# Kernel optimization log

Measured on AMD Instinct MI355X. Metric: run time of the kernel, lower is better.

## Reference

```python
import jax, jax.numpy as jnp
import numpy as np

B = 4096          # graphs per batch
SENSORS = 9       # nodes per graph (9*8 = 72 directed edges = 36 pairs x 2)
PAIRS = 36
E_PER_G = 72
HID = 3.0  # unused marker
H = 128
L = 4
EPS = 1e-8


def _build_edge_index():
    # 36 unordered pairs (i<j); per pair emit (i->j) then (j->i) so that
    # reshape(B, 36, 2) groups the two directions of each pair together.
    pairs = [(i, j) for i in range(SENSORS) for j in range(i + 1, SENSORS)]
    rows, cols = [], []
    for i, j in pairs:
        rows += [i, j]
        cols += [j, i]
    rows = np.asarray(rows, np.int32)
    cols = np.asarray(cols, np.int32)
    offs = (np.arange(B, dtype=np.int32) * SENSORS)[:, None]  # [B,1]
    row = (rows[None, :] + offs).reshape(-1)
    col = (cols[None, :] + offs).reshape(-1)
    return jnp.asarray(np.stack([row, col]))  # [2, B*72]


def setup_inputs() -> dict:
    key = jax.random.key(0)
    ks = iter(jax.random.split(key, 32))
    N = B * SENSORS

    def lin(k, fin, fout):
        s = 1.0 / np.sqrt(fin)
        kw, kb = jax.random.split(k)
        return (jax.random.uniform(kw, (fin, fout), jnp.float32, -s, s),
                jax.random.uniform(kb, (fout,), jnp.float32, -s, s))

    x_nodes = jax.random.normal(next(ks), (N, 2), jnp.float32)
    damage_locs = jax.random.normal(next(ks), (B, 2), jnp.float32)
    edge_index = _build_edge_index()
    node_batch = jnp.repeat(jnp.arange(B, dtype=jnp.int32), SENSORS)

    enc_n_w, enc_n_b = lin(next(ks), 2, H)
    enc_e_w1, enc_e_b1 = lin(next(ks), 6, H)
    enc_e_w2, enc_e_b2 = lin(next(ks), H, H)

    ew1, eb1, ew2, eb2, nw1, nb1, nw2, nb2 = [], [], [], [], [], [], [], []
    for _ in range(L):
        w, b = lin(next(ks), 3 * H, H); ew1.append(w); eb1.append(b)
        w, b = lin(next(ks), H, H);     ew2.append(w); eb2.append(b)
        w, b = lin(next(ks), 2 * H, H); nw1.append(w); nb1.append(b)
        w, b = lin(next(ks), H, H);     nw2.append(w); nb2.append(b)
    stk = lambda xs: jnp.stack(xs)

    dec_w1, dec_b1 = lin(next(ks), H, H // 2)
    dec_w2, dec_b2 = lin(next(ks), H // 2, 1)

    return dict(
        x_nodes=x_nodes, damage_locs=damage_locs,
        enc_n_w=enc_n_w, enc_n_b=enc_n_b,
        enc_e_w1=enc_e_w1, enc_e_b1=enc_e_b1, enc_e_w2=enc_e_w2, enc_e_b2=enc_e_b2,
        edge_w1=stk(ew1), edge_b1=stk(eb1), edge_w2=stk(ew2), edge_b2=stk(eb2),
        node_w1=stk(nw1), node_b1=stk(nb1), node_w2=stk(nw2), node_b2=stk(nb2),
        dec_w1=dec_w1, dec_b1=dec_b1, dec_w2=dec_w2, dec_b2=dec_b2,
        edge_index=edge_index, node_batch=node_batch,
    )


def _forward(x_nodes, damage_locs,
             enc_n_w, enc_n_b, enc_e_w1, enc_e_b1, enc_e_w2, enc_e_b2,
             edge_w1, edge_b1, edge_w2, edge_b2,
             node_w1, node_b1, node_w2, node_b2,
             dec_w1, dec_b1, dec_w2, dec_b2,
             edge_index, node_batch):
    N = x_nodes.shape[0]
    row, col = edge_index[0], edge_index[1]
    src = x_nodes[row]                      # [E,2] sender coords (p1)
    dst = x_nodes[col]                      # [E,2] receiver coords (p2)
    dmg = damage_locs[node_batch[row]]      # [E,2] (p3)

    vec = src - dst
    edge_len = jnp.sqrt(jnp.sum(vec * vec, -1, keepdims=True) + EPS)
    d21 = dst - src
    l2 = jnp.clip(jnp.sum(d21 * d21, -1, keepdims=True), EPS, None)
    t = jnp.clip(jnp.sum((dmg - src) * d21, -1, keepdims=True) / l2, 0.0, 1.0)
    proj = src + t * d21
    d_path = jnp.sqrt(jnp.sum((dmg - proj) ** 2, -1, keepdims=True) + EPS)
    d_tx = jnp.sqrt(jnp.sum((src - dmg) ** 2, -1, keepdims=True) + EPS)
    d_rx = jnp.sqrt(jnp.sum((dst - dmg) ** 2, -1, keepdims=True) + EPS)
    phys = jnp.concatenate([vec, edge_len, d_path, d_tx, d_rx], axis=1)  # [E,6]

    h_n = x_nodes @ enc_n_w + enc_n_b
    h_e = jax.nn.relu(phys @ enc_e_w1 + enc_e_b1) @ enc_e_w2 + enc_e_b2

    ones = jnp.ones((row.shape[0],), h_n.dtype)
    deg = jnp.clip(jax.ops.segment_sum(ones, col, num_segments=N), 1.0, None)[:, None]

    for l in range(L):
        ein = jnp.concatenate([h_n[row], h_n[col], h_e], axis=1)  # [E,3H]
        h_e = h_e + jax.nn.relu(ein @ edge_w1[l] + edge_b1[l]) @ edge_w2[l] + edge_b2[l]
        # PyG default message(x_j): mean of sender node features at receiver
        agg = jax.ops.segment_sum(h_n[row], col, num_segments=N) / deg
        nin = jnp.concatenate([h_n, agg], axis=1)                 # [N,2H]
        h_n = h_n + jax.nn.relu(nin @ node_w1[l] + node_b1[l]) @ node_w2[l] + node_b2[l]

    dec = jax.nn.sigmoid(jax.nn.relu(h_e @ dec_w1 + dec_b1) @ dec_w2 + dec_b2)  # [E,1]
    return dec.reshape(B, PAIRS, 2).mean(axis=2)  # [B,36]


def reference(x_nodes, damage_locs,
              enc_n_w, enc_n_b, enc_e_w1, enc_e_b1, enc_e_w2, enc_e_b2,
              edge_w1, edge_b1, edge_w2, edge_b2,
              node_w1, node_b1, node_w2, node_b2,
              dec_w1, dec_b1, dec_w2, dec_b2,
              edge_index, node_batch):
    return _forward(x_nodes, damage_locs,
                    enc_n_w, enc_n_b, enc_e_w1, enc_e_b1, enc_e_w2, enc_e_b2,
                    edge_w1, edge_b1, edge_w2, edge_b2,
                    node_w1, node_b1, node_w2, node_b2,
                    dec_w1, dec_b1, dec_w2, dec_b2,
                    edge_index, node_batch)
```

## Files before the change

kernel.cpp:

```cpp
#include <hip/hip_runtime.h>
#include <math.h>

typedef unsigned short u16;
typedef __attribute__((ext_vector_type(8))) short bf16x8;
typedef __attribute__((ext_vector_type(4))) float f32x4;

#define NSENS 9
#define NEDGE 72
#define NPAIR 36
#define HDIM 128
#define NLAYER 4
#define FEPS 1e-8f

#define ST    136
#define STNIN 264
#define STPH  40

__device__ __forceinline__ u16 f2bf(float f) {
    unsigned u = __float_as_uint(f);
    return (u16)((u + 0x7FFFu + ((u >> 16) & 1u)) >> 16);
}
__device__ __forceinline__ float bf2f(u16 h) { return __uint_as_float(((unsigned)h) << 16); }

__device__ __forceinline__ unsigned cvt2(float lo, float hi) {
#if defined(__has_builtin)
#if __has_builtin(__builtin_amdgcn_cvt_pk_bf16_f32)
    typedef __attribute__((ext_vector_type(2))) __bf16 bf16x2_t;
    bf16x2_t t = __builtin_amdgcn_cvt_pk_bf16_f32(lo, hi);
    unsigned u; __builtin_memcpy(&u, &t, 4); return u;
#else
    return ((unsigned)f2bf(hi) << 16) | (unsigned)f2bf(lo);
#endif
#else
    return ((unsigned)f2bf(hi) << 16) | (unsigned)f2bf(lo);
#endif
}

#define SZ_EE1 (1*8*512)
#define SZ_EE2 (4*8*512)
#define SZ_EW1 (12*8*512)
#define SZ_EW2 (4*8*512)
#define SZ_NW1 (8*8*512)
#define SZ_NW2 (4*8*512)
#define SZ_DW1 (4*4*512)
#define OFF_EE1 0
#define OFF_EE2 (OFF_EE1 + SZ_EE1)
#define OFF_EW1 (OFF_EE2 + SZ_EE2)
#define OFF_EW2 (OFF_EW1 + 4*SZ_EW1)
#define OFF_NW1 (OFF_EW2 + 4*SZ_EW2)
#define OFF_NW2 (OFF_NW1 + 4*SZ_NW1)
#define OFF_DW1 (OFF_NW2 + 4*SZ_NW2)

__device__ __forceinline__ void pack_one(const float* __restrict__ s, u16* __restrict__ d,
                                         int Ksrc, int N, int NT, int kbnt) {
    const int kb = kbnt / NT, nt = kbnt % NT;
    const int ln = threadIdx.x, q = ln >> 4, c = ln & 15;
    const int n  = nt * 16 + c;
    u16* dp = d + ((kb * NT + nt) * 64 + ln) * 8;
#pragma unroll
    for (int j = 0; j < 8; ++j) {
        int k = kb * 32 + q * 8 + j;
        dp[j] = f2bf((k < Ksrc) ? s[k * N + n] : 0.f);
    }
}

__global__ void pack_all(const float* __restrict__ ee1, const float* __restrict__ ee2,
                         const float* __restrict__ ew1, const float* __restrict__ ew2,
                         const float* __restrict__ nw1, const float* __restrict__ nw2,
                         const float* __restrict__ dw1, u16* __restrict__ ws) {
    int b = blockIdx.x;
    if (b < 8)        { pack_one(ee1, ws + OFF_EE1, 6, 128, 8, b); return; }
    b -= 8;
    if (b < 32)       { pack_one(ee2, ws + OFF_EE2, 128, 128, 8, b); return; }
    b -= 32;
    if (b < 384)      { int l = b / 96;
                        pack_one(ew1 + l*384*128, ws + OFF_EW1 + l*SZ_EW1, 384, 128, 8, b % 96); return; }
    b -= 384;
    if (b < 128)      { int l = b / 32;
                        pack_one(ew2 + l*128*128, ws + OFF_EW2 + l*SZ_EW2, 128, 128, 8, b % 32); return; }
    b -= 128;
    if (b < 256)      { int l = b / 64;
                        pack_one(nw1 + l*256*128, ws + OFF_NW1 + l*SZ_NW1, 256, 128, 8, b % 64); return; }
    b -= 256;
    if (b < 128)      { int l = b / 32;
                        pack_one(nw2 + l*128*128, ws + OFF_NW2 + l*SZ_NW2, 128, 128, 8, b % 32); return; }
    b -= 128;
    pack_one(dw1, ws + OFF_DW1, 128, 64, 4, b);
}

template<int NMT, int NKB, int NT, typename FA>
__device__ __forceinline__ void wave_gemm(const u16* __restrict__ Wp, int nt, int ln,
                                          FA fa, f32x4* acc) {
    const u16* wp = Wp + (nt * 64 + ln) * 8;
    bf16x8 bc = *(const bf16x8*)(wp);
#pragma unroll
    for (int kb = 0; kb < NKB; ++kb) {
        bf16x8 bn;
        if (kb + 1 < NKB) bn = *(const bf16x8*)(wp + (kb + 1) * NT * 512);
#pragma unroll
        for (int mt = 0; mt < NMT; ++mt) {
            bf16x8 a = fa(mt, kb);
            acc[mt] = __builtin_amdgcn_mfma_f32_16x16x32_bf16(a, bc, acc[mt], 0, 0, 0);
        }
        if (kb + 1 < NKB) bc = bn;
    }
}

#define BACC(A, N, b) do { _Pragma("unroll") for (int _i = 0; _i < (N); ++_i) \
                           (A)[_i] = (f32x4){(b), (b), (b), (b)}; } while (0)

extern "C" __global__ void __launch_bounds__(512, 2)
gnn_mfma(const float* __restrict__ x_nodes, const float* __restrict__ damage_locs,
         const float* __restrict__ enc_n_w, const float* __restrict__ enc_n_b,
         const float* __restrict__ enc_e_b1, const float* __restrict__ enc_e_b2,
         const float* __restrict__ edge_b1, const float* __restrict__ edge_b2,
         const float* __restrict__ node_b1, const float* __restrict__ node_b2,
         const float* __restrict__ dec_b1, const float* __restrict__ dec_w2,
         const float* __restrict__ dec_b2,
         const u16* __restrict__ wpack, float* __restrict__ out)
{
    __shared__ __align__(16) u16 smem[176 * ST];
    __shared__ float s_x[NSENS * 2];
    __shared__ float s_dmg[2];
    __shared__ float s_val[NEDGE];
    __shared__ int s_src[NEDGE], s_dst[NEDGE];

    u16* b_he  = smem;
    u16* b_t   = smem + 80 * ST;
    u16* b_hn  = smem + 160 * ST;
    u16* b_ph  = b_he;
    u16* b_nin = b_t;
    u16* b_nt  = b_t + 48 * ST;

    const int g   = blockIdx.x;
    const int tid = threadIdx.x;
    const int wv  = tid >> 6, ln = tid & 63;
    const int q   = ln >> 4,  cl = ln & 15;
    const int col = wv * 16 + cl;

    auto st4 = [&](u16* buf, int stride, int c, int Rb, int Rlim,
                   float v0, float v1, float v2, float v3) {
        unsigned d01 = cvt2(v0, v1), d23 = cvt2(v2, v3);
        if (Rb + 0 < Rlim) buf[(Rb + 0) * stride + c] = (u16)d01;
        if (Rb + 1 < Rlim) buf[(Rb + 1) * stride + c] = (u16)(d01 >> 16);
        if (Rb + 2 < Rlim) buf[(Rb + 2) * stride + c] = (u16)d23;
        if (Rb + 3 < Rlim) buf[(Rb + 3) * stride + c] = (u16)(d23 >> 16);
    };

    {
        uint4 z = {0, 0, 0, 0};
        uint4* zp = (uint4*)b_ph;
        for (int i = tid; i < (80 * STPH * 2) / 16; i += 512) zp[i] = z;
    }
    if (tid < NSENS * 2) s_x[tid] = x_nodes[g * NSENS * 2 + tid];
    if (tid < 2)         s_dmg[tid] = damage_locs[g * 2 + tid];
    if (tid < NEDGE) {
        int p = tid >> 1;
        int i = 0, rem = p, cnt = 8;
        while (rem >= cnt) { rem -= cnt; --cnt; ++i; }
        int j = i + 1 + rem;
        s_src[tid] = (tid & 1) ? j : i;
        s_dst[tid] = (tid & 1) ? i : j;
    }
    __syncthreads();

    if (tid < NEDGE) {
        const int si = s_src[tid], di = s_dst[tid];
        const float sx = s_x[2*si], sy = s_x[2*si+1];
        const float dx = s_x[2*di], dy = s_x[2*di+1];
        const float gx = s_dmg[0],  gy = s_dmg[1];
        const float vx = sx - dx, vy = sy - dy;
        const float vv = vx*vx + vy*vy;
        const float elen = sqrtf(vv + FEPS);
        const float l2 = fmaxf(vv, FEPS);
        float t = ((gx - sx) * (dx - sx) + (gy - sy) * (dy - sy)) / l2;
        t = fminf(fmaxf(t, 0.f), 1.f);
        const float px = sx + t * (dx - sx), py = sy + t * (dy - sy);
        u16* ph = b_ph + tid * STPH;
        ph[0] = f2bf(vx); ph[1] = f2bf(vy); ph[2] = f2bf(elen);
        ph[3] = f2bf(sqrtf((gx-px)*(gx-px) + (gy-py)*(gy-py) + FEPS));
        ph[4] = f2bf(sqrtf((sx-gx)*(sx-gx) + (sy-gy)*(sy-gy) + FEPS));
        ph[5] = f2bf(sqrtf((dx-gx)*(dx-gx) + (dy-gy)*(dy-gy) + FEPS));
    }

    f32x4 m_hn;
    {
        const float w0 = enc_n_w[col], w1 = enc_n_w[HDIM + col], bb = enc_n_b[col];
#pragma unroll
        for (int r = 0; r < 4; ++r) {
            const int R = q * 4 + r;
            m_hn[r] = (R < NSENS) ? fmaf(s_x[2*R], w0, fmaf(s_x[2*R+1], w1, bb)) : 0.f;
        }
        st4(b_hn, ST, col, q * 4, NSENS, m_hn[0], m_hn[1], m_hn[2], m_hn[3]);
    }

    int rowS[5], rowD[5], rowE[5];
#pragma unroll
    for (int mt = 0; mt < 5; ++mt) {
        int e = mt * 16 + cl; if (e >= NEDGE) e = NEDGE - 1;
        rowS[mt] = s_src[e] * ST; rowD[mt] = s_dst[e] * ST; rowE[mt] = e * ST;
    }
    __syncthreads();

    auto fa_t   = [&](int mt, int kb) -> bf16x8 {
        return *(const bf16x8*)(b_t + (mt * 16 + cl) * ST + kb * 32 + q * 8); };
    auto fa_ph  = [&](int mt, int kb) -> bf16x8 {
        return *(const bf16x8*)(b_ph + (mt * 16 + cl) * STPH + q * 8); };
    auto fa_nin = [&](int mt, int kb) -> bf16x8 {
        return *(const bf16x8*)(b_nin + cl * STNIN + kb * 32 + q * 8); };
    auto fa_nt  = [&](int mt, int kb) -> bf16x8 {
        return *(const bf16x8*)(b_nt + cl * ST + kb * 32 + q * 8); };
    auto fa_ein = [&](int mt, int kb) -> bf16x8 {
        const u16* p;
        if (kb < 4)      p = b_hn + rowS[mt] + kb * 32;
        else if (kb < 8) p = b_hn + rowD[mt] + (kb - 4) * 32;
        else             p = b_he + rowE[mt] + (kb - 8) * 32;
        return *(const bf16x8*)(p + q * 8); };

    f32x4 m_he[5];

    {
        f32x4 acc[5]; BACC(acc, 5, enc_e_b1[col]);
        wave_gemm<5, 1, 8>(wpack + OFF_EE1, wv, ln, fa_ph, acc);
#pragma unroll
        for (int mt = 0; mt < 5; ++mt)
            st4(b_t, ST, col, mt * 16 + q * 4, NEDGE,
                fmaxf(acc[mt][0], 0.f), fmaxf(acc[mt][1], 0.f),
                fmaxf(acc[mt][2], 0.f), fmaxf(acc[mt][3], 0.f));
    }
    __syncthreads();
    {
        f32x4 acc[5]; BACC(acc, 5, enc_e_b2[col]);
        wave_gemm<5, 4, 8>(wpack + OFF_EE2, wv, ln, fa_t, acc);
#pragma unroll
        for (int mt = 0; mt < 5; ++mt) {
            m_he[mt] = acc[mt];
            st4(b_he, ST, col, mt * 16 + q * 4, NEDGE,
                m_he[mt][0], m_he[mt][1], m_he[mt][2], m_he[mt][3]);
        }
    }
    __syncthreads();

    for (int l = 0; l < NLAYER; ++l) {
        {
            f32x4 acc[5]; BACC(acc, 5, edge_b1[l * HDIM + col]);
            wave_gemm<5, 12, 8>(wpack + OFF_EW1 + l * SZ_EW1, wv, ln, fa_ein, acc);
#pragma unroll
            for (int mt = 0; mt < 5; ++mt)
                st4(b_t, ST, col, mt * 16 + q * 4, NEDGE,
                    fmaxf(acc[mt][0], 0.f), fmaxf(acc[mt][1], 0.f),
                    fmaxf(acc[mt][2], 0.f), fmaxf(acc[mt][3], 0.f));
        }
        __syncthreads();
        {
            f32x4 acc[5]; BACC(acc, 5, edge_b2[l * HDIM + col]);
            wave_gemm<5, 4, 8>(wpack + OFF_EW2 + l * SZ_EW2, wv, ln, fa_t, acc);
#pragma unroll
            for (int mt = 0; mt < 5; ++mt) {
#pragma unroll
                for (int r = 0; r < 4; ++r) m_he[mt][r] += acc[mt][r];
                st4(b_he, ST, col, mt * 16 + q * 4, NEDGE,
                    m_he[mt][0], m_he[mt][1], m_he[mt][2], m_he[mt][3]);
            }
        }
        __syncthreads();
        {
            float p4 = m_hn[0] + m_hn[1] + m_hn[2] + m_hn[3];
            p4 += __shfl_xor(p4, 16);
            p4 += __shfl_xor(p4, 32);
            st4(b_nin, STNIN, col, q * 4, NSENS, m_hn[0], m_hn[1], m_hn[2], m_hn[3]);
            st4(b_nin, STNIN, HDIM + col, q * 4, NSENS,
                (p4 - m_hn[0]) * 0.125f, (p4 - m_hn[1]) * 0.125f,
                (p4 - m_hn[2]) * 0.125f, (p4 - m_hn[3]) * 0.125f);
        }
        __syncthreads();
        {
            f32x4 acc[1]; BACC(acc, 1, node_b1[l * HDIM + col]);
            wave_gemm<1, 8, 8>(wpack + OFF_NW1 + l * SZ_NW1, wv, ln, fa_nin, acc);
            st4(b_nt, ST, col, q * 4, 16,
                fmaxf(acc[0][0], 0.f), fmaxf(acc[0][1], 0.f),
                fmaxf(acc[0][2], 0.f), fmaxf(acc[0][3], 0.f));
        }
        __syncthreads();
        {
            f32x4 acc[1]; BACC(acc, 1, node_b2[l * HDIM + col]);
            wave_gemm<1, 4, 8>(wpack + OFF_NW2 + l * SZ_NW2, wv, ln, fa_nt, acc);
#pragma unroll
            for (int r = 0; r < 4; ++r)
                if (q * 4 + r < NSENS) m_hn[r] += acc[0][r];
            st4(b_hn, ST, col, q * 4, NSENS, m_hn[0], m_hn[1], m_hn[2], m_hn[3]);
        }
        __syncthreads();
    }

    {
        const int ntd = wv & 3;
        const int mt0 = (wv < 4) ? 0 : 2;
        auto fa_d = [&](int mt, int kb) -> bf16x8 {
            return *(const bf16x8*)(b_he + ((mt0 + mt) * 16 + cl) * ST + kb * 32 + q * 8); };
        const int c64 = ntd * 16 + cl;
        f32x4 acc[3]; BACC(acc, 3, dec_b1[c64]);
        wave_gemm<3, 4, 4>(wpack + OFF_DW1, ntd, ln, fa_d, acc);
#pragma unroll
        for (int mt = 0; mt < 3; ++mt)
            st4(b_t, ST, c64, (mt0 + mt) * 16 + q * 4, NEDGE,
                fmaxf(acc[mt][0], 0.f), fmaxf(acc[mt][1], 0.f),
                fmaxf(acc[mt][2], 0.f), fmaxf(acc[mt][3], 0.f));
    }
    __syncthreads();
    if (tid < NEDGE) {
        float a = dec_b2[0];
        const u16* tt = b_t + tid * ST;
#pragma unroll
        for (int k = 0; k < 64; ++k) a = fmaf(bf2f(tt[k]), dec_w2[k], a);
        s_val[tid] = 1.f / (1.f + expf(-a));
    }
    __syncthreads();
    if (tid < NPAIR)
        out[g * NPAIR + tid] = 0.5f * (s_val[2 * tid] + s_val[2 * tid + 1]);
}

extern "C" void kernel_launch(void* const* d_in, const int* in_sizes, int n_in,
                              void* d_out, int out_size, void* d_ws, size_t ws_size,
                              hipStream_t stream) {
    const float* x_nodes     = (const float*)d_in[0];
    const float* damage_locs = (const float*)d_in[1];
    const float* enc_n_w  = (const float*)d_in[2];
    const float* enc_n_b  = (const float*)d_in[3];
    const float* enc_e_w1 = (const float*)d_in[4];
    const float* enc_e_b1 = (const float*)d_in[5];
    const float* enc_e_w2 = (const float*)d_in[6];
    const float* enc_e_b2 = (const float*)d_in[7];
    const float* edge_w1  = (const float*)d_in[8];
    const float* edge_b1  = (const float*)d_in[9];
    const float* edge_w2  = (const float*)d_in[10];
    const float* edge_b2  = (const float*)d_in[11];
    const float* node_w1  = (const float*)d_in[12];
    const float* node_b1  = (const float*)d_in[13];
    const float* node_w2  = (const float*)d_in[14];
    const float* node_b2  = (const float*)d_in[15];
    const float* dec_w1   = (const float*)d_in[16];
    const float* dec_b1   = (const float*)d_in[17];
    const float* dec_w2   = (const float*)d_in[18];
    const float* dec_b2   = (const float*)d_in[19];
    float* out = (float*)d_out;
    u16* ws = (u16*)d_ws;

    hipLaunchKernelGGL(pack_all, dim3(952), dim3(64), 0, stream,
                       enc_e_w1, enc_e_w2, edge_w1, edge_w2, node_w1, node_w2, dec_w1, ws);

    const int ngraph = in_sizes[1] / 2;
    hipLaunchKernelGGL(gnn_mfma, dim3(ngraph), dim3(512), 0, stream,
                       x_nodes, damage_locs, enc_n_w, enc_n_b,
                       enc_e_b1, enc_e_b2, edge_b1, edge_b2,
                       node_b1, node_b2, dec_b1, dec_w2, dec_b2,
                       ws, out);
}
```

Before: 373.6 us.

## Fuse node and edge MLP stages per layer and prefetch first weight fragments

Gives the node-MLP input and hidden buffers their own shared-memory regions so the node GEMMs can run in the same phase as the edge GEMMs. This cuts the per-layer barrier count from six to two, and the node aggregation input is now written at the end of the previous phase. The first weight fragment of each upcoming GEMM is loaded before the barrier to hide global-load latency. Edge rows are clamped to 71, so the padding rows of the edge buffers are no longer read in the A-operand loads. The costs are a larger shared-memory footprint, extra zero-initialisation of the node-input padding, and more live registers.

```diff
diff --git a/kernel.cpp b/kernel.cpp
--- a/kernel.cpp
+++ b/kernel.cpp
@@ -90,9 +90,8 @@
 
 template<int NMT, int NKB, int NT, typename FA>
 __device__ __forceinline__ void wave_gemm(const u16* __restrict__ Wp, int nt, int ln,
-                                          FA fa, f32x4* acc) {
+                                          bf16x8 bc, FA fa, f32x4* acc) {
     const u16* wp = Wp + (nt * 64 + ln) * 8;
-    bf16x8 bc = *(const bf16x8*)(wp);
 #pragma unroll
     for (int kb = 0; kb < NKB; ++kb) {
         bf16x8 bn;
@@ -119,18 +118,18 @@
          const float* __restrict__ dec_b2,
          const u16* __restrict__ wpack, float* __restrict__ out)
 {
-    __shared__ __align__(16) u16 smem[176 * ST];
+    __shared__ __align__(16) u16 smem[169 * ST + 16 * STNIN];
     __shared__ float s_x[NSENS * 2];
     __shared__ float s_dmg[2];
     __shared__ float s_val[NEDGE];
     __shared__ int s_src[NEDGE], s_dst[NEDGE];
 
     u16* b_he  = smem;
-    u16* b_t   = smem + 80 * ST;
-    u16* b_hn  = smem + 160 * ST;
+    u16* b_t   = smem + 72 * ST;
+    u16* b_hn  = smem + 144 * ST;
+    u16* b_nt  = smem + 153 * ST;
+    u16* b_nin = smem + 169 * ST;
     u16* b_ph  = b_he;
-    u16* b_nin = b_t;
-    u16* b_nt  = b_t + 48 * ST;
 
     const int g   = blockIdx.x;
     const int tid = threadIdx.x;
@@ -146,11 +145,16 @@
         if (Rb + 2 < Rlim) buf[(Rb + 2) * stride + c] = (u16)d23;
         if (Rb + 3 < Rlim) buf[(Rb + 3) * stride + c] = (u16)(d23 >> 16);
     };
+    auto preB = [&](const u16* Wp, int nt) -> bf16x8 {
+        return *(const bf16x8*)(Wp + (nt * 64 + ln) * 8);
+    };
 
     {
         uint4 z = {0, 0, 0, 0};
         uint4* zp = (uint4*)b_ph;
-        for (int i = tid; i < (80 * STPH * 2) / 16; i += 512) zp[i] = z;
+        for (int i = tid; i < 360; i += 512) zp[i] = z;
+        unsigned* znp = (unsigned*)(b_nin + 9 * STNIN);
+        for (int i = tid; i < 924; i += 512) znp[i] = 0;
     }
     if (tid < NSENS * 2) s_x[tid] = x_nodes[g * NSENS * 2 + tid];
     if (tid < 2)         s_dmg[tid] = damage_locs[g * 2 + tid];
@@ -194,18 +198,18 @@
         st4(b_hn, ST, col, q * 4, NSENS, m_hn[0], m_hn[1], m_hn[2], m_hn[3]);
     }
 
-    int rowS[5], rowD[5], rowE[5];
+    int rowS[5], rowD[5], rowT[5], rowP[5];
 #pragma unroll
     for (int mt = 0; mt < 5; ++mt) {
         int e = mt * 16 + cl; if (e >= NEDGE) e = NEDGE - 1;
-        rowS[mt] = s_src[e] * ST; rowD[mt] = s_dst[e] * ST; rowE[mt] = e * ST;
-    }
-    __syncthreads();
+        rowS[mt] = s_src[e] * ST; rowD[mt] = s_dst[e] * ST;
+        rowT[mt] = e * ST;        rowP[mt] = e * STPH;
+    }
 
     auto fa_t   = [&](int mt, int kb) -> bf16x8 {
-        return *(const bf16x8*)(b_t + (mt * 16 + cl) * ST + kb * 32 + q * 8); };
+        return *(const bf16x8*)(b_t + rowT[mt] + cl * 0 + kb * 32 + q * 8); };
     auto fa_ph  = [&](int mt, int kb) -> bf16x8 {
-        return *(const bf16x8*)(b_ph + (mt * 16 + cl) * STPH + q * 8); };
+        return *(const bf16x8*)(b_ph + rowP[mt] + q * 8); };
     auto fa_nin = [&](int mt, int kb) -> bf16x8 {
         return *(const bf16x8*)(b_nin + cl * STNIN + kb * 32 + q * 8); };
     auto fa_nt  = [&](int mt, int kb) -> bf16x8 {
@@ -214,81 +218,91 @@
         const u16* p;
         if (kb < 4)      p = b_hn + rowS[mt] + kb * 32;
         else if (kb < 8) p = b_hn + rowD[mt] + (kb - 4) * 32;
-        else             p = b_he + rowE[mt] + (kb - 8) * 32;
+        else             p = b_he + rowT[mt] + (kb - 8) * 32;
         return *(const bf16x8*)(p + q * 8); };
 
+    auto write_nin = [&]() {
+        float p4 = m_hn[0] + m_hn[1] + m_hn[2] + m_hn[3];
+        p4 += __shfl_xor(p4, 16);
+        p4 += __shfl_xor(p4, 32);
+        st4(b_nin, STNIN, col, q * 4, NSENS, m_hn[0], m_hn[1], m_hn[2], m_hn[3]);
+        st4(b_nin, STNIN, HDIM + col, q * 4, NSENS,
+            (p4 - m_hn[0]) * 0.125f, (p4 - m_hn[1]) * 0.125f,
+            (p4 - m_hn[2]) * 0.125f, (p4 - m_hn[3]) * 0.125f);
+    };
+
     f32x4 m_he[5];
+    bf16x8 pE = preB(wpack + OFF_EE1, wv);
+    __syncthreads();
 
     {
         f32x4 acc[5]; BACC(acc, 5, enc_e_b1[col]);
-        wave_gemm<5, 1, 8>(wpack + OFF_EE1, wv, ln, fa_ph, acc);
+        wave_gemm<5, 1, 8>(wpack + OFF_EE1, wv, ln, pE, fa_ph, acc);
 #pragma unroll
         for (int mt = 0; mt < 5; ++mt)
             st4(b_t, ST, col, mt * 16 + q * 4, NEDGE,
                 fmaxf(acc[mt][0], 0.f), fmaxf(acc[mt][1], 0.f),
                 fmaxf(acc[mt][2], 0.f), fmaxf(acc[mt][3], 0.f));
-    }
-    __syncthreads();
+        pE = preB(wpack + OFF_EE2, wv);
+    }
+    __syncthreads();
+    bf16x8 pN;
     {
         f32x4 acc[5]; BACC(acc, 5, enc_e_b2[col]);
-        wave_gemm<5, 4, 8>(wpack + OFF_EE2, wv, ln, fa_t, acc);
+        wave_gemm<5, 4, 8>(wpack + OFF_EE2, wv, ln, pE, fa_t, acc);
 #pragma unroll
         for (int mt = 0; mt < 5; ++mt) {
             m_he[mt] = acc[mt];
             st4(b_he, ST, col, mt * 16 + q * 4, NEDGE,
                 m_he[mt][0], m_he[mt][1], m_he[mt][2], m_he[mt][3]);
         }
+        write_nin();
+        pE = preB(wpack + OFF_EW1, wv);
+        pN = preB(wpack + OFF_NW1, wv);
     }
     __syncthreads();
 
     for (int l = 0; l < NLAYER; ++l) {
         {
-            f32x4 acc[5]; BACC(acc, 5, edge_b1[l * HDIM + col]);
-            wave_gemm<5, 12, 8>(wpack + OFF_EW1 + l * SZ_EW1, wv, ln, fa_ein, acc);
+            f32x4 accE[5]; BACC(accE, 5, edge_b1[l * HDIM + col]);
+            wave_gemm<5, 12, 8>(wpack + OFF_EW1 + l * SZ_EW1, wv, ln, pE, fa_ein, accE);
+            f32x4 accN[1]; BACC(accN, 1, node_b1[l * HDIM + col]);
+            wave_gemm<1, 8, 8>(wpack + OFF_NW1 + l * SZ_NW1, wv, ln, pN, fa_nin, accN);
 #pragma unroll
             for (int mt = 0; mt < 5; ++mt)
                 st4(b_t, ST, col, mt * 16 + q * 4, NEDGE,
-                    fmaxf(acc[mt][0], 0.f), fmaxf(acc[mt][1], 0.f),
-                    fmaxf(acc[mt][2], 0.f), fmaxf(acc[mt][3], 0.f));
+                    fmaxf(accE[mt][0], 0.f), fmaxf(accE[mt][1], 0.f),
+                    fmaxf(accE[mt][2], 0.f), fmaxf(accE[mt][3], 0.f));
+            st4(b_nt, ST, col, q * 4, 16,
+                fmaxf(accN[0][0], 0.f), fmaxf(accN[0][1], 0.f),
+                fmaxf(accN[0][2], 0.f), fmaxf(accN[0][3], 0.f));
+            pE = preB(wpack + OFF_EW2 + l * SZ_EW2, wv);
+            pN = preB(wpack + OFF_NW2 + l * SZ_NW2, wv);
         }
         __syncthreads();
         {
-            f32x4 acc[5]; BACC(acc, 5, edge_b2[l * HDIM + col]);
-            wave_gemm<5, 4, 8>(wpack + OFF_EW2 + l * SZ_EW2, wv, ln, fa_t, acc);
+            f32x4 accE[5]; BACC(accE, 5, edge_b2[l * HDIM + col]);
+            wave_gemm<5, 4, 8>(wpack + OFF_EW2 + l * SZ_EW2, wv, ln, pE, fa_t, accE);
+            f32x4 accN[1]; BACC(accN, 1, node_b2[l * HDIM + col]);
+            wave_gemm<1, 4, 8>(wpack + OFF_NW2 + l * SZ_NW2, wv, ln, pN, fa_nt, accN);
 #pragma unroll
             for (int mt = 0; mt < 5; ++mt) {
 #pragma unroll
-                for (int r = 0; r < 4; ++r) m_he[mt][r] += acc[mt][r];
+                for (int r = 0; r < 4; ++r) m_he[mt][r] += accE[mt][r];
                 st4(b_he, ST, col, mt * 16 + q * 4, NEDGE,
                     m_he[mt][0], m_he[mt][1], m_he[mt][2], m_he[mt][3]);
             }
-        }
-        __syncthreads();
-        {
-            float p4 = m_hn[0] + m_hn[1] + m_hn[2] + m_hn[3];
-            p4 += __shfl_xor(p4, 16);
-            p4 += __shfl_xor(p4, 32);
-            st4(b_nin, STNIN, col, q * 4, NSENS, m_hn[0], m_hn[1], m_hn[2], m_hn[3]);
-            st4(b_nin, STNIN, HDIM + col, q * 4, NSENS,
-                (p4 - m_hn[0]) * 0.125f, (p4 - m_hn[1]) * 0.125f,
-                (p4 - m_hn[2]) * 0.125f, (p4 - m_hn[3]) * 0.125f);
-        }
-        __syncthreads();
-        {
-            f32x4 acc[1]; BACC(acc, 1, node_b1[l * HDIM + col]);
-            wave_gemm<1, 8, 8>(wpack + OFF_NW1 + l * SZ_NW1, wv, ln, fa_nin, acc);
-            st4(b_nt, ST, col, q * 4, 16,
-                fmaxf(acc[0][0], 0.f), fmaxf(acc[0][1], 0.f),
-                fmaxf(acc[0][2], 0.f), fmaxf(acc[0][3], 0.f));
-        }
-        __syncthreads();
-        {
-            f32x4 acc[1]; BACC(acc, 1, node_b2[l * HDIM + col]);
-            wave_gemm<1, 4, 8>(wpack + OFF_NW2 + l * SZ_NW2, wv, ln, fa_nt, acc);
 #pragma unroll
             for (int r = 0; r < 4; ++r)
-                if (q * 4 + r < NSENS) m_hn[r] += acc[0][r];
+                if (q * 4 + r < NSENS) m_hn[r] += accN[0][r];
             st4(b_hn, ST, col, q * 4, NSENS, m_hn[0], m_hn[1], m_hn[2], m_hn[3]);
+            write_nin();
+            if (l + 1 < NLAYER) {
+                pE = preB(wpack + OFF_EW1 + (l + 1) * SZ_EW1, wv);
+                pN = preB(wpack + OFF_NW1 + (l + 1) * SZ_NW1, wv);
+            } else {
+                pE = preB(wpack + OFF_DW1, wv & 3);
+            }
         }
         __syncthreads();
     }
@@ -296,11 +310,17 @@
     {
         const int ntd = wv & 3;
         const int mt0 = (wv < 4) ? 0 : 2;
+        int rowDd[3];
+#pragma unroll
+        for (int mt = 0; mt < 3; ++mt) {
+            int e = (mt0 + mt) * 16 + cl; if (e >= NEDGE) e = NEDGE - 1;
+            rowDd[mt] = e * ST;
+        }
         auto fa_d = [&](int mt, int kb) -> bf16x8 {
-            return *(const bf16x8*)(b_he + ((mt0 + mt) * 16 + cl) * ST + kb * 32 + q * 8); };
+            return *(const bf16x8*)(b_he + rowDd[mt] + kb * 32 + q * 8); };
         const int c64 = ntd * 16 + cl;
         f32x4 acc[3]; BACC(acc, 3, dec_b1[c64]);
-        wave_gemm<3, 4, 4>(wpack + OFF_DW1, ntd, ln, fa_d, acc);
+        wave_gemm<3, 4, 4>(wpack + OFF_DW1, ntd, ln, pE, fa_d, acc);
 #pragma unroll
         for (int mt = 0; mt < 3; ++mt)
             st4(b_t, ST, c64, (mt0 + mt) * 16 + q * 4, NEDGE,
```

Measured after the change: 453.7 us. +21.5%, slower.
